# Kernel optimization log

Hardware: AMD Instinct MI355X
Metric: run time of the kernel (lower is better)

## Reference

```python
import jax, jax.numpy as jnp
import numpy as np

B, C, W, H = 4, 256, 64, 64
CQ = C // 8  # query/key channels = 32


def setup_inputs() -> dict:
    key = jax.random.key(0)
    ks = jax.random.split(key, 8)
    s = 0.02
    return {
        "x": jax.random.normal(ks[0], (B, C, W, H), dtype=jnp.float32),
        "wq": jax.random.normal(ks[1], (CQ, C), dtype=jnp.float32) * s,
        "bq": jnp.zeros((CQ,), dtype=jnp.float32),
        "wk": jax.random.normal(ks[2], (CQ, C), dtype=jnp.float32) * s,
        "bk": jnp.zeros((CQ,), dtype=jnp.float32),
        "wv": jax.random.normal(ks[3], (C, C), dtype=jnp.float32) * s,
        "bv": jnp.zeros((C,), dtype=jnp.float32),
        "gamma": jnp.zeros((1,), dtype=jnp.float32),
    }


def reference(x, wq, bq, wk, bk, wv, bv, gamma):
    b, c, w, h = x.shape
    n = w * h
    xf = x.reshape(b, c, n)  # [B, C, N]
    # 1x1 convs == per-pixel linear projections
    q = jnp.einsum("oc,bcn->bon", wq, xf) + bq[None, :, None]  # [B, CQ, N]
    k = jnp.einsum("oc,bcn->bon", wk, xf) + bk[None, :, None]  # [B, CQ, N]
    v = jnp.einsum("oc,bcn->bon", wv, xf) + bv[None, :, None]  # [B, C, N]
    # energy[b, i, j] = <q[:, i], k[:, j]>  (i = query pos, j = key pos)
    energy = jnp.einsum("bci,bcj->bij", q, k)  # [B, N, N]
    attention = jax.nn.softmax(energy, axis=-1)  # softmax over keys
    # out[b, c, i] = sum_j v[b, c, j] * attention[b, i, j]
    out = jnp.einsum("bcj,bij->bci", v, attention).reshape(b, c, w, h)
    out = gamma * out + x
    return out, attention
```

## Files before the change

### kernel.cpp

```cpp
#include <hip/hip_runtime.h>

#define BB 4
#define CC 256
#define CQ 32
#define NN 4096

typedef __attribute__((ext_vector_type(8))) short bf16x8;
typedef __attribute__((ext_vector_type(16))) float f32x16;

__device__ __forceinline__ unsigned short f2bf(float f) {
    unsigned int u = __float_as_uint(f);
    unsigned int r = (u + 0x7fffu + ((u >> 16) & 1u)) >> 16;
    return (unsigned short)r;
}

__global__ __launch_bounds__(128) void qk_proj_kernel(
    const float* __restrict__ x,
    const float* __restrict__ wq, const float* __restrict__ bq,
    const float* __restrict__ wk, const float* __restrict__ bk,
    unsigned short* __restrict__ Qtb, unsigned short* __restrict__ Ktb,
    float* __restrict__ out)
{
    const int n   = blockIdx.x * 128 + threadIdx.x;
    const int grp = blockIdx.y;
    const int b   = blockIdx.z;
    const bool isQ = (grp < 4);
    const bool doCopy = (grp == 0);
    const int o0 = (grp & 3) * 8;

    const float* w    = isQ ? wq : wk;
    const float* bias = isQ ? bq : bk;

    float acc[8];
    #pragma unroll
    for (int u = 0; u < 8; ++u) acc[u] = bias[o0 + u];

    const float* xp = x + (size_t)b * CC * NN + n;
    float* op = out + (size_t)b * CC * NN + n;
    const float* wp = w + (size_t)o0 * CC;
    #pragma unroll 8
    for (int c = 0; c < CC; ++c) {
        float xv = xp[(size_t)c * NN];
        if (doCopy) op[(size_t)c * NN] = xv;
        #pragma unroll
        for (int u = 0; u < 8; ++u) acc[u] += wp[u * CC + c] * xv;
    }

    unsigned int pk[4];
    #pragma unroll
    for (int j = 0; j < 4; ++j)
        pk[j] = (unsigned int)f2bf(acc[2 * j]) | ((unsigned int)f2bf(acc[2 * j + 1]) << 16);

    unsigned short* dst = (isQ ? Qtb : Ktb) + ((size_t)b * NN + n) * CQ;
    *reinterpret_cast<uint4*>(dst + o0) = make_uint4(pk[0], pk[1], pk[2], pk[3]);
}

__global__ __launch_bounds__(256) void v_proj_kernel(
    const float* __restrict__ x,
    const float* __restrict__ wv, const float* __restrict__ bv,
    const float* __restrict__ gamma,
    float* __restrict__ Vt)
{
    if (gamma[0] == 0.f) return;
    for (int task = blockIdx.x; task < 2048; task += 256) {
        const int n  = (task & 15) * 256 + threadIdx.x;
        const int c0 = ((task >> 4) & 31) * 8;
        const int b  = task >> 9;

        float acc[8];
        #pragma unroll
        for (int u = 0; u < 8; ++u) acc[u] = 0.f;

        const float* xp = x + (size_t)b * CC * NN + n;
        #pragma unroll 4
        for (int c = 0; c < CC; ++c) {
            float xv = xp[(size_t)c * NN];
            #pragma unroll
            for (int u = 0; u < 8; ++u) acc[u] += wv[(size_t)(c0 + u) * CC + c] * xv;
        }
        #pragma unroll
        for (int u = 0; u < 8; ++u)
            Vt[((size_t)b * NN + n) * CC + c0 + u] = acc[u] + bv[c0 + u];
    }
}

__global__ __launch_bounds__(512, 4) void attn_kernel(
    const unsigned short* __restrict__ Qtb,
    const unsigned short* __restrict__ Ktb,
    float* __restrict__ att)
{
    __shared__ float red_s[8][32];
    __shared__ float rowls[32];
    __shared__ float tr[8][32][33];

    const int tid  = threadIdx.x;
    const int w    = tid >> 6;
    const int lane = tid & 63;
    const int l31  = lane & 31;
    const int h    = lane >> 5;

    const int flat = blockIdx.x;
    const int orig = (flat >> 3) + ((flat & 7) << 6);
    const int b    = orig >> 7;
    const int i0   = (orig & 127) * 32;

    const unsigned short* qb = Qtb + ((size_t)b * NN + i0 + l31) * CQ;
    const bf16x8 a0 = *reinterpret_cast<const bf16x8*>(qb + h * 8);
    const bf16x8 a1 = *reinterpret_cast<const bf16x8*>(qb + (h + 2) * 8);

    const unsigned short* kf = Ktb + ((size_t)b * NN + w * 512 + l31) * CQ;

    float s = 0.f;
    {
        bf16x8 nb0 = *reinterpret_cast<const bf16x8*>(kf + h * 8);
        bf16x8 nb1 = *reinterpret_cast<const bf16x8*>(kf + (h + 2) * 8);
        #pragma unroll
        for (int u = 0; u < 16; ++u) {
            bf16x8 b0 = nb0, b1 = nb1;
            if (u < 15) {
                const unsigned short* kp = kf + (size_t)(u + 1) * 32 * CQ;
                nb0 = *reinterpret_cast<const bf16x8*>(kp + h * 8);
                nb1 = *reinterpret_cast<const bf16x8*>(kp + (h + 2) * 8);
            }
            f32x16 acc{};
            acc = __builtin_amdgcn_mfma_f32_32x32x16_bf16(b0, a0, acc, 0, 0, 0);
            acc = __builtin_amdgcn_mfma_f32_32x32x16_bf16(b1, a1, acc, 0, 0, 0);
            float p0 = 0.f, p1 = 0.f;
            #pragma unroll
            for (int q = 0; q < 16; q += 2) {
                p0 += __expf(acc[q]);
                p1 += __expf(acc[q + 1]);
            }
            s += p0 + p1;
        }
    }
    s += __shfl_xor(s, 32, 64);
    if (h == 0) red_s[w][l31] = s;
    __syncthreads();
    if (tid < 32) {
        float t = red_s[0][tid];
        #pragma unroll
        for (int ww = 1; ww < 8; ++ww) t += red_s[ww][tid];
        rowls[tid] = -__logf(t);
    }
    __syncthreads();
    const float lis = rowls[l31];

    float* abase = att + ((size_t)b * NN + i0) * NN + w * 512;
    {
        bf16x8 nb0 = *reinterpret_cast<const bf16x8*>(kf + h * 8);
        bf16x8 nb1 = *reinterpret_cast<const bf16x8*>(kf + (h + 2) * 8);
        #pragma unroll
        for (int u = 0; u < 16; ++u) {
            bf16x8 b0 = nb0, b1 = nb1;
            if (u < 15) {
                const unsigned short* kp = kf + (size_t)(u + 1) * 32 * CQ;
                nb0 = *reinterpret_cast<const bf16x8*>(kp + h * 8);
                nb1 = *reinterpret_cast<const bf16x8*>(kp + (h + 2) * 8);
            }
            f32x16 acc{};
            acc = __builtin_amdgcn_mfma_f32_32x32x16_bf16(b0, a0, acc, 0, 0, 0);
            acc = __builtin_amdgcn_mfma_f32_32x32x16_bf16(b1, a1, acc, 0, 0, 0);
            #pragma unroll
            for (int q = 0; q < 16; ++q) {
                const int kc = (q & 3) + 8 * (q >> 2) + 4 * h;
                tr[w][kc][l31] = __expf(acc[q] + lis);
            }
            #pragma unroll
            for (int k = 0; k < 16; ++k) {
                const int row = 2 * k + h;
                abase[(size_t)row * NN + u * 32 + l31] = tr[w][l31][row];
            }
        }
    }
}

__global__ __launch_bounds__(256) void pv_kernel(
    const float* __restrict__ att, const float* __restrict__ Vt,
    const float* __restrict__ gamma, float* __restrict__ Pt)
{
    if (gamma[0] == 0.f) return;
    const size_t total = (size_t)BB * NN * CC;
    for (size_t idx = (size_t)blockIdx.x * 256 + threadIdx.x; idx < total;
         idx += (size_t)1024 * 256) {
        const int c = (int)(idx % CC);
        const size_t bn = idx / CC;
        const int i = (int)(bn % NN);
        const int b = (int)(bn / NN);

        const float* arow = att + ((size_t)b * NN + i) * NN;
        const float* vcol = Vt + (size_t)b * NN * CC + c;
        float acc = 0.f;
        for (int j = 0; j < NN; ++j) acc += arow[j] * vcol[(size_t)j * CC];
        Pt[idx] = acc;
    }
}

__global__ __launch_bounds__(256) void out_kernel(
    const float* __restrict__ x, const float* __restrict__ Pt,
    const float* __restrict__ gamma, float* __restrict__ out)
{
    const float g = gamma[0];
    if (g == 0.f) return;
    const size_t total4 = (size_t)BB * CC * NN / 4;
    for (size_t t = (size_t)blockIdx.x * 256 + threadIdx.x; t < total4;
         t += (size_t)512 * 256) {
        const size_t i4 = t * 4;
        float4 v = *reinterpret_cast<const float4*>(x + i4);
        #pragma unroll
        for (int e = 0; e < 4; ++e) {
            const size_t idx = i4 + e;
            const int n = (int)(idx % NN);
            const size_t bc = idx / NN;
            const int c = (int)(bc % CC);
            const int bb = (int)(bc / CC);
            (&v.x)[e] += g * Pt[((size_t)bb * NN + n) * CC + c];
        }
        *reinterpret_cast<float4*>(out + i4) = v;
    }
}

extern "C" void kernel_launch(void* const* d_in, const int* in_sizes, int n_in,
                              void* d_out, int out_size, void* d_ws, size_t ws_size,
                              hipStream_t stream)
{
    const float* x     = (const float*)d_in[0];
    const float* wq    = (const float*)d_in[1];
    const float* bq    = (const float*)d_in[2];
    const float* wk    = (const float*)d_in[3];
    const float* bk    = (const float*)d_in[4];
    const float* wv    = (const float*)d_in[5];
    const float* bv    = (const float*)d_in[6];
    const float* gamma = (const float*)d_in[7];

    float* out = (float*)d_out;
    float* att = out + (size_t)BB * CC * NN;

    unsigned short* Qtb = (unsigned short*)d_ws;
    unsigned short* Ktb = Qtb + (size_t)BB * NN * CQ;
    float* Vt = (float*)(Ktb + (size_t)BB * NN * CQ);
    float* Pt = Vt + (size_t)BB * NN * CC;

    qk_proj_kernel<<<dim3(NN / 128, 8, BB), 128, 0, stream>>>(x, wq, bq, wk, bk, Qtb, Ktb, out);
    v_proj_kernel<<<dim3(256), 256, 0, stream>>>(x, wv, bv, gamma, Vt);
    attn_kernel<<<dim3(512), 512, 0, stream>>>(Qtb, Ktb, att);
    pv_kernel<<<dim3(1024), 256, 0, stream>>>(att, Vt, gamma, Pt);
    out_kernel<<<dim3(512), 256, 0, stream>>>(x, Pt, gamma, out);
}
```

Measured before the change: 104.3 us.

## Stage full 32x512 attention tile in LDS for wide coalesced float4 stores

```diff
diff --git a/kernel.cpp b/kernel.cpp
--- a/kernel.cpp
+++ b/kernel.cpp
@@ -12,6 +12,10 @@
     unsigned int u = __float_as_uint(f);
     unsigned int r = (u + 0x7fffu + ((u >> 16) & 1u)) >> 16;
     return (unsigned short)r;
+}
+
+__device__ __forceinline__ void lds_barrier() {
+    asm volatile("s_waitcnt lgkmcnt(0)\n\ts_barrier" ::: "memory");
 }
 
 __global__ __launch_bounds__(128) void qk_proj_kernel(
@@ -91,7 +95,7 @@
 {
     __shared__ float red_s[8][32];
     __shared__ float rowls[32];
-    __shared__ float tr[8][32][33];
+    __shared__ __align__(16) float sbuf[32][517];
 
     const int tid  = threadIdx.x;
     const int w    = tid >> 6;
@@ -109,7 +113,6 @@
     const bf16x8 a1 = *reinterpret_cast<const bf16x8*>(qb + (h + 2) * 8);
 
     const unsigned short* kf = Ktb + ((size_t)b * NN + w * 512 + l31) * CQ;
-
     float s = 0.f;
     {
         bf16x8 nb0 = *reinterpret_cast<const bf16x8*>(kf + h * 8);
@@ -146,32 +149,63 @@
     __syncthreads();
     const float lis = rowls[l31];
 
-    float* abase = att + ((size_t)b * NN + i0) * NN + w * 512;
-    {
-        bf16x8 nb0 = *reinterpret_cast<const bf16x8*>(kf + h * 8);
-        bf16x8 nb1 = *reinterpret_cast<const bf16x8*>(kf + (h + 2) * 8);
-        #pragma unroll
-        for (int u = 0; u < 16; ++u) {
-            bf16x8 b0 = nb0, b1 = nb1;
-            if (u < 15) {
-                const unsigned short* kp = kf + (size_t)(u + 1) * 32 * CQ;
-                nb0 = *reinterpret_cast<const bf16x8*>(kp + h * 8);
-                nb1 = *reinterpret_cast<const bf16x8*>(kp + (h + 2) * 8);
-            }
+    const unsigned short* kfw = Ktb + ((size_t)b * NN + w * 64 + l31) * CQ;
+    float* arow = att + ((size_t)b * NN + i0) * NN;
+
+    bf16x8 c00 = *reinterpret_cast<const bf16x8*>(kfw + h * 8);
+    bf16x8 c01 = *reinterpret_cast<const bf16x8*>(kfw + (h + 2) * 8);
+    bf16x8 c10 = *reinterpret_cast<const bf16x8*>(kfw + (size_t)32 * CQ + h * 8);
+    bf16x8 c11 = *reinterpret_cast<const bf16x8*>(kfw + (size_t)32 * CQ + (h + 2) * 8);
+
+    #pragma unroll
+    for (int m = 0; m < 8; ++m) {
+        {
             f32x16 acc{};
-            acc = __builtin_amdgcn_mfma_f32_32x32x16_bf16(b0, a0, acc, 0, 0, 0);
-            acc = __builtin_amdgcn_mfma_f32_32x32x16_bf16(b1, a1, acc, 0, 0, 0);
-            #pragma unroll
-            for (int q = 0; q < 16; ++q) {
-                const int kc = (q & 3) + 8 * (q >> 2) + 4 * h;
-                tr[w][kc][l31] = __expf(acc[q] + lis);
-            }
-            #pragma unroll
-            for (int k = 0; k < 16; ++k) {
-                const int row = 2 * k + h;
-                abase[(size_t)row * NN + u * 32 + l31] = tr[w][l31][row];
-            }
-        }
+            acc = __builtin_amdgcn_mfma_f32_32x32x16_bf16(c00, a0, acc, 0, 0, 0);
+            acc = __builtin_amdgcn_mfma_f32_32x32x16_bf16(c01, a1, acc, 0, 0, 0);
+            #pragma unroll
+            for (int g2 = 0; g2 < 4; ++g2) {
+                float4 e4;
+                e4.x = __expf(acc[4 * g2 + 0] + lis);
+                e4.y = __expf(acc[4 * g2 + 1] + lis);
+                e4.z = __expf(acc[4 * g2 + 2] + lis);
+                e4.w = __expf(acc[4 * g2 + 3] + lis);
+                *reinterpret_cast<float4*>(&sbuf[l31][w * 64 + 8 * g2 + 4 * h]) = e4;
+            }
+        }
+        {
+            f32x16 acc{};
+            acc = __builtin_amdgcn_mfma_f32_32x32x16_bf16(c10, a0, acc, 0, 0, 0);
+            acc = __builtin_amdgcn_mfma_f32_32x32x16_bf16(c11, a1, acc, 0, 0, 0);
+            #pragma unroll
+            for (int g2 = 0; g2 < 4; ++g2) {
+                float4 e4;
+                e4.x = __expf(acc[4 * g2 + 0] + lis);
+                e4.y = __expf(acc[4 * g2 + 1] + lis);
+                e4.z = __expf(acc[4 * g2 + 2] + lis);
+                e4.w = __expf(acc[4 * g2 + 3] + lis);
+                *reinterpret_cast<float4*>(&sbuf[l31][w * 64 + 32 + 8 * g2 + 4 * h]) = e4;
+            }
+        }
+        if (m < 7) {
+            const unsigned short* kp = kfw + (size_t)(m + 1) * 512 * CQ;
+            c00 = *reinterpret_cast<const bf16x8*>(kp + h * 8);
+            c01 = *reinterpret_cast<const bf16x8*>(kp + (h + 2) * 8);
+            c10 = *reinterpret_cast<const bf16x8*>(kp + (size_t)32 * CQ + h * 8);
+            c11 = *reinterpret_cast<const bf16x8*>(kp + (size_t)32 * CQ + (h + 2) * 8);
+        }
+        lds_barrier();
+
+        #pragma unroll
+        for (int i = 0; i < 4; ++i) {
+            const int row = i * 8 + w;
+            float4 v0 = *reinterpret_cast<const float4*>(&sbuf[row][4 * lane]);
+            float4 v1 = *reinterpret_cast<const float4*>(&sbuf[row][256 + 4 * lane]);
+            float* dst = arow + (size_t)row * NN + m * 512 + 4 * lane;
+            *reinterpret_cast<float4*>(dst)       = v0;
+            *reinterpret_cast<float4*>(dst + 256) = v1;
+        }
+        lds_barrier();
     }
 }
 
```

After: 111.6 us. +6.9%, slower.
